# Kernel tuning notes

Hardware: AMD Instinct MI355X
Metric: run time of the kernel (lower is better)

Reference implementation:

```python
import jax, jax.numpy as jnp
import numpy as np

B, IN_F, OUT_F, K = 8192, 1024, 4096, 2
S = 64  # sqrt(OUT_F)


def setup_inputs() -> dict:
    key = jax.random.key(0)
    k1, k2, k3, k4 = jax.random.split(key, 4)
    x = jax.random.normal(k1, (B, IN_F), dtype=jnp.float32)
    y = jax.random.normal(k2, (B, OUT_F), dtype=jnp.float32)
    weight = jax.random.normal(k3, (OUT_F, IN_F), dtype=jnp.float32) * (1.0 / np.sqrt(IN_F))
    bias = jax.random.normal(k4, (OUT_F,), dtype=jnp.float32) * (1.0 / np.sqrt(IN_F))
    return {"x": x, "y": y, "weight": weight, "bias": bias}


def reference(x, y, weight, bias):
    # fused GEMM + bias + residual add epilogue
    out_lin = jnp.einsum('bk,nk->bn', x, weight) + bias + y  # (B, OUT_F)
    feat = out_lin.reshape(B, S, S)
    # AvgPool2d(kernel=K, stride=K)
    s_out = S // K
    pooled = feat.reshape(B, s_out, K, s_out, K).mean(axis=(2, 4))  # (B, s_out, s_out)
    # divide by global mean of the pooled map
    mean_val = pooled.mean()
    normed = pooled / mean_val
    return normed[:, None, :, :]  # (B, 1, s_out, s_out)
```

## Files before the change

### kernel.cpp

```cpp
#include <hip/hip_runtime.h>
#include <stdint.h>


#define KDIM 1024
#define NP   1024
#define BM 256
#define BN 128
#define BK 64
#define NBLK 256

typedef __bf16 bf16x8 __attribute__((ext_vector_type(8)));
typedef float f32x4 __attribute__((ext_vector_type(4)));

__device__ __forceinline__ unsigned f2bf(float f) {
  union { float f; unsigned u; } v; v.f = f;
  unsigned r = v.u + 0x7fffu + ((v.u >> 16) & 1u);
  return r >> 16;
}

__device__ __forceinline__ void gload_lds16(const void* g, void* l) {
  __builtin_amdgcn_global_load_lds(
      (const __attribute__((address_space(1))) void*)g,
      (__attribute__((address_space(3))) void*)l, 16, 0, 0);
}

__global__ void k_prep(const float* __restrict__ x, const float* __restrict__ W,
                       const float* __restrict__ bias,
                       unsigned short* __restrict__ xb, unsigned short* __restrict__ wp,
                       float* __restrict__ biasp) {
  int b = blockIdx.x;
  int t = threadIdx.x;
  if (b < 4096) {
    int i = b * 256 + t;
    const float4* x4 = (const float4*)x;
    float4 a = x4[i * 2], c = x4[i * 2 + 1];
    uint4 o;
    o.x = f2bf(a.x) | (f2bf(a.y) << 16);
    o.y = f2bf(a.z) | (f2bf(a.w) << 16);
    o.z = f2bf(c.x) | (f2bf(c.y) << 16);
    o.w = f2bf(c.z) | (f2bf(c.w) << 16);
    ((uint4*)xb)[i] = o;
  } else {
    int o = b - 4096;
    int r0 = ((o >> 5) << 7) + ((o & 31) << 1);
    const float4* W4 = (const float4*)W;
    float4 w0 = W4[(r0) * 256 + t];
    float4 w1 = W4[(r0 + 1) * 256 + t];
    float4 w2 = W4[(r0 + 64) * 256 + t];
    float4 w3 = W4[(r0 + 65) * 256 + t];
    float ax = 0.25f * (w0.x + w1.x + w2.x + w3.x);
    float ay = 0.25f * (w0.y + w1.y + w2.y + w3.y);
    float az = 0.25f * (w0.z + w1.z + w2.z + w3.z);
    float aw = 0.25f * (w0.w + w1.w + w2.w + w3.w);
    uint2 pk;
    pk.x = f2bf(ax) | (f2bf(ay) << 16);
    pk.y = f2bf(az) | (f2bf(aw) << 16);
    ((uint2*)wp)[o * 256 + t] = pk;
    if (t == 0)
      biasp[o] = 0.25f * (bias[r0] + bias[r0 + 1] + bias[r0 + 64] + bias[r0 + 65]);
  }
}

__global__ __launch_bounds__(512, 2) void k_gemm(
    const unsigned short* __restrict__ xb, const unsigned short* __restrict__ wp,
    const float* __restrict__ biasp, const float* __restrict__ y,
    float* __restrict__ out, float* __restrict__ partials) {
  __shared__ char smem[98304];

  int bid = blockIdx.x;
  int wg = (bid & 7) * 32 + (bid >> 3);
  int bm0 = (wg >> 3) * BM;
  int bn0 = (wg & 7) * BN;

  int tid = threadIdx.x;
  int lane = tid & 63;
  int wid = tid >> 6;
  int wr = wid >> 1, wc = wid & 1;

  f32x4 acc[4][4];
#pragma unroll
  for (int i = 0; i < 4; i++)
#pragma unroll
    for (int j = 0; j < 4; j++) acc[i][j] = (f32x4)0.0f;

  int srow = tid >> 3;
  int scol = (((lane & 7) ^ (lane >> 3)) << 3);
  const unsigned short* aSrc = xb + (size_t)(bm0 + srow) * KDIM + scol;
  const unsigned short* bSrc = wp + (size_t)(bn0 + srow) * KDIM + scol;
  int ldsOff = wid * 1024;

  int rbase = (lane & 15) * 128;
  int xorv = (lane & 7) << 4;
  int cb0 = (((lane >> 4) * 16)) ^ xorv;
  int cb1 = ((64 + (lane >> 4) * 16)) ^ xorv;

#define STAGE(buf, ks)                                                         \
  {                                                                            \
    int k0 = (ks) * BK;                                                        \
    char* ab = smem + (buf) * 49152 + ldsOff;                                  \
    char* bb = smem + (buf) * 49152 + 32768 + ldsOff;                          \
    _Pragma("unroll")                                                          \
    for (int i = 0; i < 4; ++i)                                                \
      gload_lds16(aSrc + (size_t)i * 64 * KDIM + k0, ab + i * 8192);           \
    _Pragma("unroll")                                                          \
    for (int i = 0; i < 2; ++i)                                                \
      gload_lds16(bSrc + (size_t)i * 64 * KDIM + k0, bb + i * 8192);           \
  }

  STAGE(0, 0);
  for (int ks = 0; ks < 16; ++ks) {
    int cur = ks & 1;
    if (ks < 15) {
      STAGE(cur ^ 1, ks + 1);
      asm volatile("s_waitcnt vmcnt(6)" ::: "memory");
    } else {
      asm volatile("s_waitcnt vmcnt(0)" ::: "memory");
    }
    __builtin_amdgcn_s_barrier();
    asm volatile("" ::: "memory");
    const char* Ab = smem + cur * 49152;
    const char* Bb = Ab + 32768;
#pragma unroll
    for (int kk = 0; kk < 2; ++kk) {
      int cb = kk ? cb1 : cb0;
      bf16x8 af[4], bfr[4];
#pragma unroll
      for (int mi = 0; mi < 4; ++mi)
        af[mi] = *(const bf16x8*)(Ab + (wr * 64 + mi * 16) * 128 + rbase + cb);
#pragma unroll
      for (int ni = 0; ni < 4; ++ni)
        bfr[ni] = *(const bf16x8*)(Bb + (wc * 64 + ni * 16) * 128 + rbase + cb);
#pragma unroll
      for (int mi = 0; mi < 4; ++mi)
#pragma unroll
        for (int ni = 0; ni < 4; ++ni)
          acc[mi][ni] = __builtin_amdgcn_mfma_f32_16x16x32_bf16(af[mi], bfr[ni], acc[mi][ni], 0, 0, 0);
    }
    asm volatile("" ::: "memory");
    __builtin_amdgcn_s_barrier();
  }

  const float2* y2 = (const float2*)y;
  float tsum = 0.f;
  int r_l = (lane >> 4) * 4;
  int c_l = lane & 15;
#pragma unroll
  for (int mi = 0; mi < 4; ++mi) {
#pragma unroll
    for (int ni = 0; ni < 4; ++ni) {
      int col = bn0 + wc * 64 + ni * 16 + c_l;
      float bp = biasp[col];
      int y2base = ((col >> 5) << 6) + (col & 31);
#pragma unroll
      for (int j = 0; j < 4; ++j) {
        int row = bm0 + wr * 64 + mi * 16 + r_l + j;
        float2 u = y2[(size_t)row * 2048 + y2base];
        float2 v = y2[(size_t)row * 2048 + y2base + 32];
        float val = acc[mi][ni][j] + bp + 0.25f * (u.x + u.y + v.x + v.y);
        out[(size_t)row * NP + col] = val;
        tsum += val;
      }
    }
  }
#pragma unroll
  for (int off = 32; off > 0; off >>= 1) tsum += __shfl_down(tsum, off);
  float* sm = (float*)smem;
  __syncthreads();
  if (lane == 0) sm[wid] = tsum;
  __syncthreads();
  if (tid == 0)
    partials[bid] = ((sm[0] + sm[1]) + (sm[2] + sm[3])) +
                    ((sm[4] + sm[5]) + (sm[6] + sm[7]));
}

__global__ void k_norm(float* __restrict__ out, const float* __restrict__ partials) {
  __shared__ float s[256];
  int t = threadIdx.x;
  s[t] = partials[t];
  __syncthreads();
#pragma unroll
  for (int off = 128; off > 0; off >>= 1) {
    if (t < off) s[t] += s[t + off];
    __syncthreads();
  }
  float inv = 8388608.0f / s[0];
  int i = blockIdx.x * 256 + t;
  float4* o4 = (float4*)out;
  float4 v = o4[i];
  v.x *= inv; v.y *= inv; v.z *= inv; v.w *= inv;
  o4[i] = v;
}

extern "C" void kernel_launch(void* const* d_in, const int* in_sizes, int n_in,
                              void* d_out, int out_size, void* d_ws, size_t ws_size,
                              hipStream_t stream) {
  (void)in_sizes; (void)n_in; (void)out_size; (void)ws_size;
  const float* x = (const float*)d_in[0];
  const float* y = (const float*)d_in[1];
  const float* W = (const float*)d_in[2];
  const float* bias = (const float*)d_in[3];
  float* out = (float*)d_out;

  char* ws = (char*)d_ws;
  unsigned short* xb = (unsigned short*)(ws);
  unsigned short* wp = (unsigned short*)(ws + 16777216);
  float* biasp = (float*)(ws + 16777216 + 2097152);
  float* partials = (float*)(ws + 16777216 + 2097152 + 4096);

  hipLaunchKernelGGL(k_prep, dim3(5120), dim3(256), 0, stream, x, W, bias, xb, wp, biasp);
  hipLaunchKernelGGL(k_gemm, dim3(NBLK), dim3(512), 0, stream, xb, wp, biasp, y, out, partials);
  hipLaunchKernelGGL(k_norm, dim3(8192), dim3(256), 0, stream, out, partials);
}
```

Measured before the change: 69.99 us.

## Halve GEMM M-tile to 512 blocks and stage pre-norm output in fp16

Shrinks the GEMM M tile from 256 to 128, which doubles the grid to 512 blocks, cuts LDS to 64KB and drops the occupancy hint, so the work spreads across more CUs. When the workspace is large enough, the GEMM epilogue writes the un-normalised pooled values as fp16 to a scratch buffer, and the norm kernel reads them back and writes the fp32 output. This cuts the intermediate write and read traffic. In exchange, the intermediate values are rounded to fp16 before scaling, and the partial-sum reduction now reads 512 entries.

```diff
diff --git a/kernel.cpp b/kernel.cpp
--- a/kernel.cpp
+++ b/kernel.cpp
@@ -4,13 +4,13 @@
 
 #define KDIM 1024
 #define NP   1024
-#define BM 256
+#define BM 128
 #define BN 128
 #define BK 64
-#define NBLK 256
 
 typedef __bf16 bf16x8 __attribute__((ext_vector_type(8)));
 typedef float f32x4 __attribute__((ext_vector_type(4)));
+typedef _Float16 f16x4 __attribute__((ext_vector_type(4)));
 
 __device__ __forceinline__ unsigned f2bf(float f) {
   union { float f; unsigned u; } v; v.f = f;
@@ -61,14 +61,15 @@
   }
 }
 
-__global__ __launch_bounds__(512, 2) void k_gemm(
+__global__ __launch_bounds__(512) void k_gemm(
     const unsigned short* __restrict__ xb, const unsigned short* __restrict__ wp,
     const float* __restrict__ biasp, const float* __restrict__ y,
-    float* __restrict__ out, float* __restrict__ partials) {
-  __shared__ char smem[98304];
+    float* __restrict__ out, _Float16* __restrict__ ph,
+    float* __restrict__ partials, int use16) {
+  __shared__ char smem[65536];
 
   int bid = blockIdx.x;
-  int wg = (bid & 7) * 32 + (bid >> 3);
+  int wg = (bid & 7) * 64 + (bid >> 3);
   int bm0 = (wg >> 3) * BM;
   int bn0 = (wg & 7) * BN;
 
@@ -77,9 +78,9 @@
   int wid = tid >> 6;
   int wr = wid >> 1, wc = wid & 1;
 
-  f32x4 acc[4][4];
-#pragma unroll
-  for (int i = 0; i < 4; i++)
+  f32x4 acc[2][4];
+#pragma unroll
+  for (int i = 0; i < 2; i++)
 #pragma unroll
     for (int j = 0; j < 4; j++) acc[i][j] = (f32x4)0.0f;
 
@@ -97,10 +98,10 @@
 #define STAGE(buf, ks)                                                         \
   {                                                                            \
     int k0 = (ks) * BK;                                                        \
-    char* ab = smem + (buf) * 49152 + ldsOff;                                  \
-    char* bb = smem + (buf) * 49152 + 32768 + ldsOff;                          \
+    char* ab = smem + (buf) * 32768 + ldsOff;                                  \
+    char* bb = smem + (buf) * 32768 + 16384 + ldsOff;                          \
     _Pragma("unroll")                                                          \
-    for (int i = 0; i < 4; ++i)                                                \
+    for (int i = 0; i < 2; ++i)                                                \
       gload_lds16(aSrc + (size_t)i * 64 * KDIM + k0, ab + i * 8192);           \
     _Pragma("unroll")                                                          \
     for (int i = 0; i < 2; ++i)                                                \
@@ -112,26 +113,26 @@
     int cur = ks & 1;
     if (ks < 15) {
       STAGE(cur ^ 1, ks + 1);
-      asm volatile("s_waitcnt vmcnt(6)" ::: "memory");
+      asm volatile("s_waitcnt vmcnt(4)" ::: "memory");
     } else {
       asm volatile("s_waitcnt vmcnt(0)" ::: "memory");
     }
     __builtin_amdgcn_s_barrier();
     asm volatile("" ::: "memory");
-    const char* Ab = smem + cur * 49152;
-    const char* Bb = Ab + 32768;
+    const char* Ab = smem + cur * 32768;
+    const char* Bb = Ab + 16384;
 #pragma unroll
     for (int kk = 0; kk < 2; ++kk) {
       int cb = kk ? cb1 : cb0;
-      bf16x8 af[4], bfr[4];
-#pragma unroll
-      for (int mi = 0; mi < 4; ++mi)
-        af[mi] = *(const bf16x8*)(Ab + (wr * 64 + mi * 16) * 128 + rbase + cb);
+      bf16x8 af[2], bfr[4];
+#pragma unroll
+      for (int mi = 0; mi < 2; ++mi)
+        af[mi] = *(const bf16x8*)(Ab + (wr * 32 + mi * 16) * 128 + rbase + cb);
 #pragma unroll
       for (int ni = 0; ni < 4; ++ni)
         bfr[ni] = *(const bf16x8*)(Bb + (wc * 64 + ni * 16) * 128 + rbase + cb);
 #pragma unroll
-      for (int mi = 0; mi < 4; ++mi)
+      for (int mi = 0; mi < 2; ++mi)
 #pragma unroll
         for (int ni = 0; ni < 4; ++ni)
           acc[mi][ni] = __builtin_amdgcn_mfma_f32_16x16x32_bf16(af[mi], bfr[ni], acc[mi][ni], 0, 0, 0);
@@ -145,7 +146,7 @@
   int r_l = (lane >> 4) * 4;
   int c_l = lane & 15;
 #pragma unroll
-  for (int mi = 0; mi < 4; ++mi) {
+  for (int mi = 0; mi < 2; ++mi) {
 #pragma unroll
     for (int ni = 0; ni < 4; ++ni) {
       int col = bn0 + wc * 64 + ni * 16 + c_l;
@@ -153,11 +154,13 @@
       int y2base = ((col >> 5) << 6) + (col & 31);
 #pragma unroll
       for (int j = 0; j < 4; ++j) {
-        int row = bm0 + wr * 64 + mi * 16 + r_l + j;
+        int row = bm0 + wr * 32 + mi * 16 + r_l + j;
         float2 u = y2[(size_t)row * 2048 + y2base];
         float2 v = y2[(size_t)row * 2048 + y2base + 32];
         float val = acc[mi][ni][j] + bp + 0.25f * (u.x + u.y + v.x + v.y);
-        out[(size_t)row * NP + col] = val;
+        size_t idx = (size_t)row * NP + col;
+        if (use16) ph[idx] = (_Float16)val;
+        else out[idx] = val;
         tsum += val;
       }
     }
@@ -173,10 +176,11 @@
                     ((sm[4] + sm[5]) + (sm[6] + sm[7]));
 }
 
-__global__ void k_norm(float* __restrict__ out, const float* __restrict__ partials) {
+__global__ void k_norm(float* __restrict__ out, const _Float16* __restrict__ ph,
+                       const float* __restrict__ partials, int use16) {
   __shared__ float s[256];
   int t = threadIdx.x;
-  s[t] = partials[t];
+  s[t] = partials[t] + partials[t + 256];
   __syncthreads();
 #pragma unroll
   for (int off = 128; off > 0; off >>= 1) {
@@ -186,15 +190,25 @@
   float inv = 8388608.0f / s[0];
   int i = blockIdx.x * 256 + t;
   float4* o4 = (float4*)out;
-  float4 v = o4[i];
-  v.x *= inv; v.y *= inv; v.z *= inv; v.w *= inv;
-  o4[i] = v;
+  if (use16) {
+    f16x4 hv = ((const f16x4*)ph)[i];
+    float4 v;
+    v.x = (float)hv[0] * inv;
+    v.y = (float)hv[1] * inv;
+    v.z = (float)hv[2] * inv;
+    v.w = (float)hv[3] * inv;
+    o4[i] = v;
+  } else {
+    float4 v = o4[i];
+    v.x *= inv; v.y *= inv; v.z *= inv; v.w *= inv;
+    o4[i] = v;
+  }
 }
 
 extern "C" void kernel_launch(void* const* d_in, const int* in_sizes, int n_in,
                               void* d_out, int out_size, void* d_ws, size_t ws_size,
                               hipStream_t stream) {
-  (void)in_sizes; (void)n_in; (void)out_size; (void)ws_size;
+  (void)in_sizes; (void)n_in; (void)out_size;
   const float* x = (const float*)d_in[0];
   const float* y = (const float*)d_in[1];
   const float* W = (const float*)d_in[2];
@@ -206,8 +220,10 @@
   unsigned short* wp = (unsigned short*)(ws + 16777216);
   float* biasp = (float*)(ws + 16777216 + 2097152);
   float* partials = (float*)(ws + 16777216 + 2097152 + 4096);
+  _Float16* ph = (_Float16*)(ws + 20971520);
+  int use16 = (ws_size >= (size_t)20971520 + 16777216) ? 1 : 0;
 
   hipLaunchKernelGGL(k_prep, dim3(5120), dim3(256), 0, stream, x, W, bias, xb, wp, biasp);
-  hipLaunchKernelGGL(k_gemm, dim3(NBLK), dim3(512), 0, stream, xb, wp, biasp, y, out, partials);
-  hipLaunchKernelGGL(k_norm, dim3(8192), dim3(256), 0, stream, out, partials);
-}
+  hipLaunchKernelGGL(k_gemm, dim3(512), dim3(512), 0, stream, xb, wp, biasp, y, out, ph, partials, use16);
+  hipLaunchKernelGGL(k_norm, dim3(8192), dim3(256), 0, stream, out, ph, partials, use16);
+}
```

Result: faster. 62.13 us (-11.2%).

## Overlap residual loads with GEMM mainloop and store fp16 intermediate

Applied to the files above, without the earlier changes.

Moves the pooled residual (y) loads into the unrolled GEMM mainloop so they are issued alongside the LDS staging and consumed two tiles later, hiding their latency behind MFMA work. It also splits the LDS staging into two halves interleaved with the two MFMA sub-steps, adding explicit waitcnts, sched_barriers and priority raises. When the workspace is large enough, the unnormalized intermediate is written as fp16 to a scratch buffer and read back by the normalize kernel, halving that round-trip traffic at the cost of fp16 precision in the pre-normalization values. The extra in-flight y registers may raise register pressure.

```diff
diff --git a/kernel.cpp b/kernel.cpp
--- a/kernel.cpp
+++ b/kernel.cpp
@@ -11,6 +11,7 @@
 
 typedef __bf16 bf16x8 __attribute__((ext_vector_type(8)));
 typedef float f32x4 __attribute__((ext_vector_type(4)));
+typedef _Float16 f16x4 __attribute__((ext_vector_type(4)));
 
 __device__ __forceinline__ unsigned f2bf(float f) {
   union { float f; unsigned u; } v; v.f = f;
@@ -64,7 +65,8 @@
 __global__ __launch_bounds__(512, 2) void k_gemm(
     const unsigned short* __restrict__ xb, const unsigned short* __restrict__ wp,
     const float* __restrict__ biasp, const float* __restrict__ y,
-    float* __restrict__ out, float* __restrict__ partials) {
+    float* __restrict__ out, _Float16* __restrict__ ph,
+    float* __restrict__ partials, int use16) {
   __shared__ char smem[98304];
 
   int bid = blockIdx.x;
@@ -94,70 +96,144 @@
   int cb0 = (((lane >> 4) * 16)) ^ xorv;
   int cb1 = ((64 + (lane >> 4) * 16)) ^ xorv;
 
-#define STAGE(buf, ks)                                                         \
+  const float2* y2 = (const float2*)y;
+  int r_l = (lane >> 4) * 4;
+  int c_l = lane & 15;
+  int yrb = bm0 + wr * 64 + r_l;
+  int yb[4];
+#pragma unroll
+  for (int ni = 0; ni < 4; ++ni) {
+    int col = bn0 + wc * 64 + ni * 16 + c_l;
+    yb[ni] = ((col >> 5) << 6) + (col & 31);
+  }
+  float2 yin[2][8];
+
+#define STAGE_P1(buf, ks)                                                      \
+  {                                                                            \
+    int k0 = (ks) * BK;                                                        \
+    char* ab = smem + (buf) * 49152 + ldsOff;                                  \
+    gload_lds16(aSrc + k0, ab);                                                \
+    gload_lds16(aSrc + (size_t)64 * KDIM + k0, ab + 8192);                     \
+    gload_lds16(aSrc + (size_t)128 * KDIM + k0, ab + 16384);                   \
+  }
+#define STAGE_P2(buf, ks)                                                      \
   {                                                                            \
     int k0 = (ks) * BK;                                                        \
     char* ab = smem + (buf) * 49152 + ldsOff;                                  \
     char* bb = smem + (buf) * 49152 + 32768 + ldsOff;                          \
+    gload_lds16(aSrc + (size_t)192 * KDIM + k0, ab + 24576);                   \
+    gload_lds16(bSrc + k0, bb);                                                \
+    gload_lds16(bSrc + (size_t)64 * KDIM + k0, bb + 8192);                     \
+  }
+
+#define YLD2(slot, s, q)                                                       \
+  {                                                                            \
+    const float2* pp = y2 +                                                    \
+        (size_t)(yrb + (((q) >> 4) * 16) + ((q) & 3)) * 2048 + yb[((q) >> 2) & 3]; \
+    asm volatile("global_load_dwordx2 %0, %1, off"                             \
+                 : "=v"(yin[slot][2 * (s)]) : "v"(pp) : "memory");             \
+    asm volatile("global_load_dwordx2 %0, %1, off offset:256"                  \
+                 : "=v"(yin[slot][2 * (s) + 1]) : "v"(pp) : "memory");         \
+  }
+#define YLOAD8(slot, t)                                                        \
+  { YLD2(slot, 0, 4 * (t)) YLD2(slot, 1, 4 * (t) + 1)                          \
+    YLD2(slot, 2, 4 * (t) + 2) YLD2(slot, 3, 4 * (t) + 3) }
+#define YCONS4(slot, p)                                                        \
+  {                                                                            \
     _Pragma("unroll")                                                          \
-    for (int i = 0; i < 4; ++i)                                                \
-      gload_lds16(aSrc + (size_t)i * 64 * KDIM + k0, ab + i * 8192);           \
+    for (int s = 0; s < 4; ++s)                                                \
+      acc[(p) >> 2][(p) & 3][s] +=                                             \
+          0.25f * ((yin[slot][2 * s].x + yin[slot][2 * s].y) +                 \
+                   (yin[slot][2 * s + 1].x + yin[slot][2 * s + 1].y));         \
+  }
+
+#define FRAGS(av, bv, cbv, Ab, Bb)                                             \
+  {                                                                            \
     _Pragma("unroll")                                                          \
-    for (int i = 0; i < 2; ++i)                                                \
-      gload_lds16(bSrc + (size_t)i * 64 * KDIM + k0, bb + i * 8192);           \
-  }
-
-  STAGE(0, 0);
-  for (int ks = 0; ks < 16; ++ks) {
-    int cur = ks & 1;
-    if (ks < 15) {
-      STAGE(cur ^ 1, ks + 1);
-      asm volatile("s_waitcnt vmcnt(6)" ::: "memory");
-    } else {
-      asm volatile("s_waitcnt vmcnt(0)" ::: "memory");
-    }
-    __builtin_amdgcn_s_barrier();
-    asm volatile("" ::: "memory");
-    const char* Ab = smem + cur * 49152;
-    const char* Bb = Ab + 32768;
-#pragma unroll
-    for (int kk = 0; kk < 2; ++kk) {
-      int cb = kk ? cb1 : cb0;
-      bf16x8 af[4], bfr[4];
-#pragma unroll
-      for (int mi = 0; mi < 4; ++mi)
-        af[mi] = *(const bf16x8*)(Ab + (wr * 64 + mi * 16) * 128 + rbase + cb);
-#pragma unroll
-      for (int ni = 0; ni < 4; ++ni)
-        bfr[ni] = *(const bf16x8*)(Bb + (wc * 64 + ni * 16) * 128 + rbase + cb);
-#pragma unroll
-      for (int mi = 0; mi < 4; ++mi)
-#pragma unroll
-        for (int ni = 0; ni < 4; ++ni)
-          acc[mi][ni] = __builtin_amdgcn_mfma_f32_16x16x32_bf16(af[mi], bfr[ni], acc[mi][ni], 0, 0, 0);
-    }
-    asm volatile("" ::: "memory");
-    __builtin_amdgcn_s_barrier();
-  }
-
-  const float2* y2 = (const float2*)y;
+    for (int mi = 0; mi < 4; ++mi)                                             \
+      av[mi] = *(const bf16x8*)((Ab) + (wr * 64 + mi * 16) * 128 + rbase + (cbv)); \
+    _Pragma("unroll")                                                          \
+    for (int ni = 0; ni < 4; ++ni)                                             \
+      bv[ni] = *(const bf16x8*)((Bb) + (wc * 64 + ni * 16) * 128 + rbase + (cbv)); \
+  }
+#define MM16(av, bv)                                                           \
+  {                                                                            \
+    _Pragma("unroll")                                                          \
+    for (int mi = 0; mi < 4; ++mi)                                             \
+      _Pragma("unroll")                                                        \
+      for (int ni = 0; ni < 4; ++ni)                                           \
+        acc[mi][ni] = __builtin_amdgcn_mfma_f32_16x16x32_bf16(                 \
+            av[mi], bv[ni], acc[mi][ni], 0, 0, 0);                             \
+  }
+
+#define TILE(t, WSTR)                                                          \
+  {                                                                            \
+    asm volatile(WSTR ::: "memory");                                           \
+    __builtin_amdgcn_sched_barrier(0);                                         \
+    __builtin_amdgcn_s_barrier();                                              \
+    if ((t) >= 2) YCONS4(((t) - 2) & 1, (t) - 2);                              \
+    const char* Ab = smem + ((t) & 1) * 49152;                                 \
+    const char* Bb = Ab + 32768;                                               \
+    bf16x8 a0[4], b0[4];                                                       \
+    FRAGS(a0, b0, cb0, Ab, Bb);                                                \
+    if ((t) < 15) STAGE_P1(((t) + 1) & 1, (t) + 1);                            \
+    asm volatile("s_waitcnt lgkmcnt(0)" ::: "memory");                         \
+    __builtin_amdgcn_sched_barrier(0);                                         \
+    __builtin_amdgcn_s_setprio(1);                                             \
+    MM16(a0, b0);                                                              \
+    __builtin_amdgcn_s_setprio(0);                                             \
+    bf16x8 a1[4], b1[4];                                                       \
+    FRAGS(a1, b1, cb1, Ab, Bb);                                                \
+    if ((t) < 15) STAGE_P2(((t) + 1) & 1, (t) + 1);                            \
+    YLOAD8((t) & 1, t);                                                        \
+    asm volatile("s_waitcnt lgkmcnt(0)" ::: "memory");                         \
+    __builtin_amdgcn_sched_barrier(0);                                         \
+    __builtin_amdgcn_s_setprio(1);                                             \
+    MM16(a1, b1);                                                              \
+    __builtin_amdgcn_s_setprio(0);                                             \
+  }
+
+  STAGE_P1(0, 0);
+  STAGE_P2(0, 0);
+
+  TILE(0,  "s_waitcnt vmcnt(0)")
+  TILE(1,  "s_waitcnt vmcnt(8)")
+  TILE(2,  "s_waitcnt vmcnt(8)")
+  TILE(3,  "s_waitcnt vmcnt(8)")
+  TILE(4,  "s_waitcnt vmcnt(8)")
+  TILE(5,  "s_waitcnt vmcnt(8)")
+  TILE(6,  "s_waitcnt vmcnt(8)")
+  TILE(7,  "s_waitcnt vmcnt(8)")
+  TILE(8,  "s_waitcnt vmcnt(8)")
+  TILE(9,  "s_waitcnt vmcnt(8)")
+  TILE(10, "s_waitcnt vmcnt(8)")
+  TILE(11, "s_waitcnt vmcnt(8)")
+  TILE(12, "s_waitcnt vmcnt(8)")
+  TILE(13, "s_waitcnt vmcnt(8)")
+  TILE(14, "s_waitcnt vmcnt(8)")
+  TILE(15, "s_waitcnt vmcnt(8)")
+
+  asm volatile("s_waitcnt vmcnt(0)" ::: "memory");
+  __builtin_amdgcn_sched_barrier(0);
+  YCONS4(0, 14);
+  YCONS4(1, 15);
+
   float tsum = 0.f;
-  int r_l = (lane >> 4) * 4;
-  int c_l = lane & 15;
+  float bpv[4];
+#pragma unroll
+  for (int ni = 0; ni < 4; ++ni) bpv[ni] = biasp[bn0 + wc * 64 + ni * 16 + c_l];
 #pragma unroll
   for (int mi = 0; mi < 4; ++mi) {
 #pragma unroll
     for (int ni = 0; ni < 4; ++ni) {
       int col = bn0 + wc * 64 + ni * 16 + c_l;
-      float bp = biasp[col];
-      int y2base = ((col >> 5) << 6) + (col & 31);
 #pragma unroll
       for (int j = 0; j < 4; ++j) {
         int row = bm0 + wr * 64 + mi * 16 + r_l + j;
-        float2 u = y2[(size_t)row * 2048 + y2base];
-        float2 v = y2[(size_t)row * 2048 + y2base + 32];
-        float val = acc[mi][ni][j] + bp + 0.25f * (u.x + u.y + v.x + v.y);
-        out[(size_t)row * NP + col] = val;
+        float val = acc[mi][ni][j] + bpv[ni];
+        size_t o = (size_t)row * NP + col;
+        if (use16) ph[o] = (_Float16)val;
+        else out[o] = val;
         tsum += val;
       }
     }
@@ -173,7 +249,8 @@
                     ((sm[4] + sm[5]) + (sm[6] + sm[7]));
 }
 
-__global__ void k_norm(float* __restrict__ out, const float* __restrict__ partials) {
+__global__ void k_norm(float* __restrict__ out, const _Float16* __restrict__ ph,
+                       const float* __restrict__ partials, int use16) {
   __shared__ float s[256];
   int t = threadIdx.x;
   s[t] = partials[t];
@@ -186,15 +263,25 @@
   float inv = 8388608.0f / s[0];
   int i = blockIdx.x * 256 + t;
   float4* o4 = (float4*)out;
-  float4 v = o4[i];
-  v.x *= inv; v.y *= inv; v.z *= inv; v.w *= inv;
-  o4[i] = v;
+  if (use16) {
+    f16x4 hv = ((const f16x4*)ph)[i];
+    float4 v;
+    v.x = (float)hv[0] * inv;
+    v.y = (float)hv[1] * inv;
+    v.z = (float)hv[2] * inv;
+    v.w = (float)hv[3] * inv;
+    o4[i] = v;
+  } else {
+    float4 v = o4[i];
+    v.x *= inv; v.y *= inv; v.z *= inv; v.w *= inv;
+    o4[i] = v;
+  }
 }
 
 extern "C" void kernel_launch(void* const* d_in, const int* in_sizes, int n_in,
                               void* d_out, int out_size, void* d_ws, size_t ws_size,
                               hipStream_t stream) {
-  (void)in_sizes; (void)n_in; (void)out_size; (void)ws_size;
+  (void)in_sizes; (void)n_in; (void)out_size;
   const float* x = (const float*)d_in[0];
   const float* y = (const float*)d_in[1];
   const float* W = (const float*)d_in[2];
@@ -206,8 +293,10 @@
   unsigned short* wp = (unsigned short*)(ws + 16777216);
   float* biasp = (float*)(ws + 16777216 + 2097152);
   float* partials = (float*)(ws + 16777216 + 2097152 + 4096);
+  _Float16* ph = (_Float16*)(ws + 20971520);
+  int use16 = (ws_size >= (size_t)20971520 + 16777216) ? 1 : 0;
 
   hipLaunchKernelGGL(k_prep, dim3(5120), dim3(256), 0, stream, x, W, bias, xb, wp, biasp);
-  hipLaunchKernelGGL(k_gemm, dim3(NBLK), dim3(512), 0, stream, xb, wp, biasp, y, out, partials);
-  hipLaunchKernelGGL(k_norm, dim3(8192), dim3(256), 0, stream, out, partials);
-}
+  hipLaunchKernelGGL(k_gemm, dim3(NBLK), dim3(512), 0, stream, xb, wp, biasp, y, out, ph, partials, use16);
+  hipLaunchKernelGGL(k_norm, dim3(8192), dim3(256), 0, stream, out, ph, partials, use16);
+}
```

After: 57.46 us, median of 2. 1.22x faster.
